# Performance work log

Hardware: AMD Instinct MI355X
Metric: run time of the kernel (lower is better)

The kernel has to match this reference:

```python
import jax, jax.numpy as jnp
import numpy as np

N = 50000      # num_nodes
E = 600000     # num_edges
DIN = 3
D = 128        # hidden_dim == output_dim
H = 4          # heads
C = D // H     # per-head channels = 32
L = 3          # num_layers
NEG_SLOPE = 0.2
LN_EPS = 1e-5


def setup_inputs() -> dict:
    key = jax.random.key(0)
    ks = jax.random.split(key, 14)
    s = 1.0 / np.sqrt(D)
    return {
        "x": jax.random.normal(ks[0], (E, DIN), dtype=jnp.float32),
        "edge_index": jax.random.randint(ks[1], (2, E), 0, N, dtype=jnp.int32),
        "W_edge": jax.random.normal(ks[2], (DIN, D), dtype=jnp.float32) / np.sqrt(DIN),
        "b_edge": jnp.zeros((D,), jnp.float32),
        "W_node": jax.random.normal(ks[3], (D, D), dtype=jnp.float32) * s,
        "b_node": jnp.zeros((D,), jnp.float32),
        "lin_w": jax.random.normal(ks[4], (L, D, D), dtype=jnp.float32) * s,   # GATConv lin (bias=False)
        "att_src": jax.random.normal(ks[5], (L, H, C), dtype=jnp.float32) * s,
        "att_dst": jax.random.normal(ks[6], (L, H, C), dtype=jnp.float32) * s,
        "gat_bias": jnp.zeros((L, D), jnp.float32),
        "ln_g": jnp.ones((L, D), jnp.float32),
        "ln_b": jnp.zeros((L, D), jnp.float32),
        "num_nodes": N,
    }


def _layernorm(x, g, b):
    mu = x.mean(-1, keepdims=True)
    var = ((x - mu) ** 2).mean(-1, keepdims=True)
    return (x - mu) * jax.lax.rsqrt(var + LN_EPS) * g + b


def reference(x, edge_index, W_edge, b_edge, W_node, b_node,
              lin_w, att_src, att_dst, gat_bias, ln_g, ln_b, num_nodes):
    n = num_nodes
    row, col = edge_index[0], edge_index[1]

    # Edge -> node scatter-mean init (x has edge features, E != N)
    edge_h = x @ W_edge + b_edge                                   # [E, D]
    h = jax.ops.segment_sum(edge_h, col, num_segments=n)           # [N, D]
    cnt = jax.ops.segment_sum(jnp.ones((E,), x.dtype), col, num_segments=n)
    h = h / jnp.clip(cnt, 1.0)[:, None]
    h = h @ W_node + b_node

    # self-loops (PyG GATConv default add_self_loops=True)
    loop = jnp.arange(n, dtype=row.dtype)
    src = jnp.concatenate([row, loop])                             # [E+N]
    dst = jnp.concatenate([col, loop])

    for i in range(L):
        xh = (h @ lin_w[i]).reshape(n, H, C)                       # [N, H, C]
        a_s = (xh * att_src[i]).sum(-1)                            # [N, H]
        a_d = (xh * att_dst[i]).sum(-1)
        e = jax.nn.leaky_relu(a_s[src] + a_d[dst], NEG_SLOPE)      # [E+N, H]
        # segment softmax over incoming edges per destination node
        m = jax.ops.segment_max(e, dst, num_segments=n)            # [N, H]
        ex = jnp.exp(e - m[dst])
        denom = jax.ops.segment_sum(ex, dst, num_segments=n)       # [N, H]
        alpha = ex / denom[dst]                                    # [E+N, H]
        out = jax.ops.segment_sum(alpha[:, :, None] * xh[src], dst,
                                  num_segments=n)                  # [N, H, C]
        h_new = out.reshape(n, D) + gat_bias[i]
        h_new = _layernorm(h_new, ln_g[i], ln_b[i])
        if i < L - 1:
            h_new = jax.nn.relu(h_new)
        h = h + h_new                                              # residual (dims match)
    return h
```

## Files before the change

kernel.cpp:

```cpp
#include <hip/hip_runtime.h>
#include <hip/hip_bf16.h>
#include <math.h>

#define D 128
#define H 4
#define NEG_SLOPE 0.2f
#define LN_EPS 1e-5f
#define LDA 136
#define LDE 132

using bf16x8 = __attribute__((ext_vector_type(8))) short;
using f32x4  = __attribute__((ext_vector_type(4))) float;

__device__ __forceinline__ float lrelu(float v) {
    return v > 0.f ? v : NEG_SLOPE * v;
}
__device__ __forceinline__ unsigned short bfb(float f) {
    __hip_bfloat16 h = __float2bfloat16(f);
    return *reinterpret_cast<unsigned short*>(&h);
}

__global__ void k_count(const int* __restrict__ ei, int* __restrict__ cnt, int E) {
    int e = blockIdx.x * blockDim.x + threadIdx.x;
    if (e >= E) return;
    atomicAdd(&cnt[ei[E + e]], 1);
}

__global__ void k_scan_part(const int* __restrict__ cnt, int* __restrict__ off,
                            int* __restrict__ bsum, int N) {
    __shared__ int sm[256];
    int i = blockIdx.x * 256 + threadIdx.x;
    int v = (i < N) ? cnt[i] : 0;
    sm[threadIdx.x] = v;
    __syncthreads();
    #pragma unroll
    for (int o = 1; o < 256; o <<= 1) {
        int t = (threadIdx.x >= (unsigned)o) ? sm[threadIdx.x - o] : 0;
        __syncthreads();
        sm[threadIdx.x] += t;
        __syncthreads();
    }
    if (i < N) off[i] = sm[threadIdx.x];
    if (threadIdx.x == 255) bsum[blockIdx.x] = sm[255];
}

__global__ void k_scan_top(int* __restrict__ bsum, int* __restrict__ off,
                           int NB, int N) {
    __shared__ int sm[256];
    int v = (threadIdx.x < (unsigned)NB) ? bsum[threadIdx.x] : 0;
    sm[threadIdx.x] = v;
    __syncthreads();
    #pragma unroll
    for (int o = 1; o < 256; o <<= 1) {
        int t = (threadIdx.x >= (unsigned)o) ? sm[threadIdx.x - o] : 0;
        __syncthreads();
        sm[threadIdx.x] += t;
        __syncthreads();
    }
    if (threadIdx.x < (unsigned)NB) bsum[threadIdx.x] = sm[threadIdx.x] - v;
    if (threadIdx.x == 255) off[N] = sm[255];
}

__global__ void k_scan_add(const int* __restrict__ cnt, int* __restrict__ off,
                           const int* __restrict__ bsum, int N) {
    int i = blockIdx.x * 256 + threadIdx.x;
    if (i < N) off[i] = off[i] - cnt[i] + bsum[blockIdx.x];
}

__global__ void k_fill(const int* __restrict__ ei, const int* __restrict__ off,
                       int* __restrict__ pos, int2* __restrict__ adj2, int E) {
    int e = blockIdx.x * blockDim.x + threadIdx.x;
    if (e >= E) return;
    int dst = ei[E + e];
    int slot = off[dst] + atomicAdd(&pos[dst], 1);
    adj2[slot] = make_int2(ei[e], e);
}

__global__ __launch_bounds__(256) void k_wprep(
        const float* __restrict__ Wn, const float* __restrict__ lw,
        unsigned short* __restrict__ Wt) {
    __shared__ float Wf[32][132];
    int b = blockIdx.x, w = b >> 2, p = b & 3;
    const float* src = (w == 0) ? (Wn + (size_t)p * 32 * D)
                                : (lw + (size_t)(w - 1) * D * D + (size_t)p * 32 * D);
    int tid = threadIdx.x;
    #pragma unroll
    for (int j = 0; j < 4; j++) {
        int i = tid + j * 256;
        int r = i >> 5, q = i & 31;
        float4 v = reinterpret_cast<const float4*>(src)[i];
        *reinterpret_cast<float4*>(&Wf[r][q * 4]) = v;
    }
    __syncthreads();
    int n = tid & 127, ks = (tid >> 7) * 16;
    unsigned short t16[16];
    #pragma unroll
    for (int j = 0; j < 16; j++) t16[j] = bfb(Wf[ks + j][n]);
    unsigned short* dst = Wt + ((size_t)w * D + n) * D + p * 32 + ks;
    *reinterpret_cast<uint4*>(dst) = *reinterpret_cast<uint4*>(t16);
    *reinterpret_cast<uint4*>(dst + 8) = *reinterpret_cast<uint4*>(t16 + 8);
}

template <int MODE>
__global__ __launch_bounds__(256) void k_gemm(
        const float* __restrict__ A, const unsigned short* __restrict__ Wt,
        const float* __restrict__ bias, float* __restrict__ C,
        __hip_bfloat16* __restrict__ xhb, float* __restrict__ a_s,
        float* __restrict__ a_d, const float* __restrict__ att_s,
        const float* __restrict__ att_d,
        const float* __restrict__ x, const int2* __restrict__ adj2,
        const int* __restrict__ off,
        const float* __restrict__ W_edge, const float* __restrict__ b_edge,
        int N) {
    __shared__ __align__(16) unsigned short AsB[64 * LDA];
    __shared__ __align__(16) unsigned short WtB[128 * LDA];
    int tid = threadIdx.x;
    int n0 = blockIdx.x * 64;

    #pragma unroll
    for (int j = 0; j < 8; j++) {
        int ch = tid + j * 256;
        int r = ch >> 4, c = ch & 15;
        uint4 v = *reinterpret_cast<const uint4*>(Wt + (size_t)r * D + c * 8);
        *reinterpret_cast<uint4*>(&WtB[r * LDA + c * 8]) = v;
    }

    if (MODE == 2) {
        __shared__ float rowf[64][4];
        {
            int r = tid >> 2, t4 = tid & 3;
            int n = n0 + r;
            float s0 = 0.f, s1 = 0.f, s2 = 0.f;
            int degv = 0;
            if (n < N) {
                int beg = off[n], end = off[n + 1];
                degv = end - beg;
                for (int p = beg + t4; p < end; p += 4) {
                    const float* xr = x + (size_t)adj2[p].y * 3;
                    s0 += xr[0]; s1 += xr[1]; s2 += xr[2];
                }
            }
            s0 += __shfl_xor(s0, 1); s0 += __shfl_xor(s0, 2);
            s1 += __shfl_xor(s1, 1); s1 += __shfl_xor(s1, 2);
            s2 += __shfl_xor(s2, 1); s2 += __shfl_xor(s2, 2);
            if (t4 == 0)
                *reinterpret_cast<float4*>(rowf[r]) =
                    make_float4(s0, s1, s2, (float)degv);
        }
        __syncthreads();
        #pragma unroll
        for (int j = 0; j < 4; j++) {
            int ch = tid + j * 256;
            int r = ch >> 4, c = ch & 15;
            float4 rv = *reinterpret_cast<float4*>(rowf[r]);
            float cn = rv.w, rc = 1.f / fmaxf(cn, 1.f);
            int d0 = c * 8;
            unsigned short t8[8];
            #pragma unroll
            for (int q = 0; q < 2; q++) {
                float4 we0 = *reinterpret_cast<const float4*>(W_edge + d0 + q * 4);
                float4 we1 = *reinterpret_cast<const float4*>(W_edge + D + d0 + q * 4);
                float4 we2 = *reinterpret_cast<const float4*>(W_edge + 2 * D + d0 + q * 4);
                float4 be  = *reinterpret_cast<const float4*>(b_edge + d0 + q * 4);
                t8[q * 4 + 0] = bfb((rv.x * we0.x + rv.y * we1.x + rv.z * we2.x + cn * be.x) * rc);
                t8[q * 4 + 1] = bfb((rv.x * we0.y + rv.y * we1.y + rv.z * we2.y + cn * be.y) * rc);
                t8[q * 4 + 2] = bfb((rv.x * we0.z + rv.y * we1.z + rv.z * we2.z + cn * be.z) * rc);
                t8[q * 4 + 3] = bfb((rv.x * we0.w + rv.y * we1.w + rv.z * we2.w + cn * be.w) * rc);
            }
            *reinterpret_cast<uint4*>(&AsB[r * LDA + c * 8]) =
                *reinterpret_cast<uint4*>(t8);
        }
    } else {
        #pragma unroll
        for (int j = 0; j < 4; j++) {
            int ch = tid + j * 256;
            int r = ch >> 4, c = ch & 15;
            int n = n0 + r;
            float4 v0 = make_float4(0.f, 0.f, 0.f, 0.f), v1 = v0;
            if (n < N) {
                v0 = reinterpret_cast<const float4*>(A)[(size_t)n * 32 + c * 2];
                v1 = reinterpret_cast<const float4*>(A)[(size_t)n * 32 + c * 2 + 1];
            }
            unsigned short t8[8] = {bfb(v0.x), bfb(v0.y), bfb(v0.z), bfb(v0.w),
                                    bfb(v1.x), bfb(v1.y), bfb(v1.z), bfb(v1.w)};
            *reinterpret_cast<uint4*>(&AsB[r * LDA + c * 8]) =
                *reinterpret_cast<uint4*>(t8);
        }
    }
    __syncthreads();

    int lane = tid & 63, wv = tid >> 6;
    int lrow = lane & 15, lk = lane >> 4;
    f32x4 acc[8];
    #pragma unroll
    for (int ct = 0; ct < 8; ct++) acc[ct] = (f32x4){0.f, 0.f, 0.f, 0.f};
    int arow = wv * 16 + lrow;
    #pragma unroll
    for (int ks = 0; ks < 4; ks++) {
        bf16x8 af = *reinterpret_cast<const bf16x8*>(
            &AsB[arow * LDA + ks * 32 + lk * 8]);
        #pragma unroll
        for (int ct = 0; ct < 8; ct++) {
            bf16x8 bfr = *reinterpret_cast<const bf16x8*>(
                &WtB[(ct * 16 + lrow) * LDA + ks * 32 + lk * 8]);
            acc[ct] = __builtin_amdgcn_mfma_f32_16x16x32_bf16(af, bfr, acc[ct], 0, 0, 0);
        }
    }
    __syncthreads();

    float* Ef = reinterpret_cast<float*>(WtB);
    #pragma unroll
    for (int ct = 0; ct < 8; ct++)
        #pragma unroll
        for (int j = 0; j < 4; j++)
            Ef[(wv * 16 + lk * 4 + j) * LDE + ct * 16 + lrow] = acc[ct][j];
    __syncthreads();

    int tx = tid & 15, ty = tid >> 4;
    int c0 = tx * 8, r0 = ty * 4;
    float o[4][8];
    #pragma unroll
    for (int r = 0; r < 4; r++) {
        float4 v0 = *reinterpret_cast<const float4*>(&Ef[(r0 + r) * LDE + c0]);
        float4 v1 = *reinterpret_cast<const float4*>(&Ef[(r0 + r) * LDE + c0 + 4]);
        o[r][0] = v0.x; o[r][1] = v0.y; o[r][2] = v0.z; o[r][3] = v0.w;
        o[r][4] = v1.x; o[r][5] = v1.y; o[r][6] = v1.z; o[r][7] = v1.w;
    }

    if (MODE == 2) {
        float b[8];
        #pragma unroll
        for (int c = 0; c < 8; c++) b[c] = bias[c0 + c];
        #pragma unroll
        for (int r = 0; r < 4; r++) {
            int n = n0 + r0 + r;
            if (n >= N) continue;
            float4 o0 = make_float4(o[r][0] + b[0], o[r][1] + b[1],
                                    o[r][2] + b[2], o[r][3] + b[3]);
            float4 o1 = make_float4(o[r][4] + b[4], o[r][5] + b[5],
                                    o[r][6] + b[6], o[r][7] + b[7]);
            reinterpret_cast<float4*>(C)[(size_t)n * 32 + tx * 2] = o0;
            reinterpret_cast<float4*>(C)[(size_t)n * 32 + tx * 2 + 1] = o1;
        }
    } else {
        float ats[8], atd[8];
        #pragma unroll
        for (int c = 0; c < 8; c++) { ats[c] = att_s[c0 + c]; atd[c] = att_d[c0 + c]; }
        #pragma unroll
        for (int r = 0; r < 4; r++) {
            int n = n0 + r0 + r;
            union { uint4 v; unsigned short s[8]; } pk;
            #pragma unroll
            for (int c = 0; c < 8; c++) pk.s[c] = bfb(o[r][c]);
            float ps = 0.f, pd = 0.f;
            #pragma unroll
            for (int c = 0; c < 8; c++) { ps += o[r][c] * ats[c]; pd += o[r][c] * atd[c]; }
            ps += __shfl_xor(ps, 1); ps += __shfl_xor(ps, 2);
            pd += __shfl_xor(pd, 1); pd += __shfl_xor(pd, 2);
            if (n < N) {
                *reinterpret_cast<uint4*>(xhb + (size_t)n * D + c0) = pk.v;
                if ((tx & 3) == 0) {
                    a_s[n * H + (tx >> 2)] = ps;
                    a_d[n * H + (tx >> 2)] = pd;
                }
            }
        }
    }
}

__global__ __launch_bounds__(256) void k_gat5(
        const __hip_bfloat16* __restrict__ xhb, const int* __restrict__ off,
        const int2* __restrict__ adj2, const float* __restrict__ a_s,
        const float* __restrict__ a_d, const float* __restrict__ bias,
        const float* __restrict__ g, const float* __restrict__ bln,
        float* __restrict__ h, int N, int do_relu) {
    int wid = threadIdx.x >> 6;
    int lane = threadIdx.x & 63;
    int n = blockIdx.x * 4 + wid;
    if (n >= N) return;

    int cl = lane & 15;
    int sub = lane >> 4;
    int hb = cl >> 2;
    int c0 = cl * 8;

    int beg = off[n], end = off[n + 1];
    int deg = end - beg;
    int items = deg + 1;
    int itp = (items + 3) & ~3;

    float adA = a_d[n * H + hb];
    float den = 0.f;
    float acc[8];
    #pragma unroll
    for (int c = 0; c < 8; c++) acc[c] = 0.f;

    #pragma unroll 4
    for (int pp = sub; pp < itp; pp += 4) {
        int s = (pp < deg) ? adj2[beg + pp].x : n;
        float av = a_s[(size_t)s * H + hb];
        uint4 u = *reinterpret_cast<const uint4*>(xhb + (size_t)s * D + c0);
        float e = lrelu(av + adA);
        float wv = (pp < items) ? __expf(e) : 0.f;
        den += wv;
        float f;
        f = __uint_as_float(u.x << 16);         acc[0] += wv * f;
        f = __uint_as_float(u.x & 0xffff0000u); acc[1] += wv * f;
        f = __uint_as_float(u.y << 16);         acc[2] += wv * f;
        f = __uint_as_float(u.y & 0xffff0000u); acc[3] += wv * f;
        f = __uint_as_float(u.z << 16);         acc[4] += wv * f;
        f = __uint_as_float(u.z & 0xffff0000u); acc[5] += wv * f;
        f = __uint_as_float(u.w << 16);         acc[6] += wv * f;
        f = __uint_as_float(u.w & 0xffff0000u); acc[7] += wv * f;
    }

    #pragma unroll
    for (int c = 0; c < 8; c++) {
        acc[c] += __shfl_xor(acc[c], 16);
        acc[c] += __shfl_xor(acc[c], 32);
    }
    den += __shfl_xor(den, 16);
    den += __shfl_xor(den, 32);
    float rden = 1.0f / den;

    float4 b0 = *reinterpret_cast<const float4*>(bias + c0);
    float4 b1 = *reinterpret_cast<const float4*>(bias + c0 + 4);
    float o[8];
    o[0] = acc[0] * rden + b0.x; o[1] = acc[1] * rden + b0.y;
    o[2] = acc[2] * rden + b0.z; o[3] = acc[3] * rden + b0.w;
    o[4] = acc[4] * rden + b1.x; o[5] = acc[5] * rden + b1.y;
    o[6] = acc[6] * rden + b1.z; o[7] = acc[7] * rden + b1.w;

    float s1 = 0.f;
    #pragma unroll
    for (int c = 0; c < 8; c++) s1 += o[c];
    #pragma unroll
    for (int os = 1; os < 64; os <<= 1) s1 += __shfl_xor(s1, os);
    float mu = s1 * (1.0f / 512.0f);
    float s2 = 0.f;
    #pragma unroll
    for (int c = 0; c < 8; c++) { float dv = o[c] - mu; s2 += dv * dv; }
    #pragma unroll
    for (int os = 1; os < 64; os <<= 1) s2 += __shfl_xor(s2, os);
    float inv = rsqrtf(s2 * (1.0f / 512.0f) + LN_EPS);

    if (sub == 0) {
        float4 g0 = *reinterpret_cast<const float4*>(g + c0);
        float4 g1 = *reinterpret_cast<const float4*>(g + c0 + 4);
        float4 l0 = *reinterpret_cast<const float4*>(bln + c0);
        float4 l1 = *reinterpret_cast<const float4*>(bln + c0 + 4);
        float y[8];
        y[0] = (o[0] - mu) * inv * g0.x + l0.x;
        y[1] = (o[1] - mu) * inv * g0.y + l0.y;
        y[2] = (o[2] - mu) * inv * g0.z + l0.z;
        y[3] = (o[3] - mu) * inv * g0.w + l0.w;
        y[4] = (o[4] - mu) * inv * g1.x + l1.x;
        y[5] = (o[5] - mu) * inv * g1.y + l1.y;
        y[6] = (o[6] - mu) * inv * g1.z + l1.z;
        y[7] = (o[7] - mu) * inv * g1.w + l1.w;
        if (do_relu) {
            #pragma unroll
            for (int c = 0; c < 8; c++) y[c] = fmaxf(y[c], 0.f);
        }
        float4 h0 = *reinterpret_cast<float4*>(h + (size_t)n * D + c0);
        float4 h1 = *reinterpret_cast<float4*>(h + (size_t)n * D + c0 + 4);
        h0.x += y[0]; h0.y += y[1]; h0.z += y[2]; h0.w += y[3];
        h1.x += y[4]; h1.y += y[5]; h1.z += y[6]; h1.w += y[7];
        *reinterpret_cast<float4*>(h + (size_t)n * D + c0) = h0;
        *reinterpret_cast<float4*>(h + (size_t)n * D + c0 + 4) = h1;
    }
}

extern "C" void kernel_launch(void* const* d_in, const int* in_sizes, int n_in,
                              void* d_out, int out_size, void* d_ws, size_t ws_size,
                              hipStream_t stream) {
    const float* x       = (const float*)d_in[0];
    const int*   ei      = (const int*)  d_in[1];
    const float* W_edge  = (const float*)d_in[2];
    const float* b_edge  = (const float*)d_in[3];
    const float* W_node  = (const float*)d_in[4];
    const float* b_node  = (const float*)d_in[5];
    const float* lin_w   = (const float*)d_in[6];
    const float* att_src = (const float*)d_in[7];
    const float* att_dst = (const float*)d_in[8];
    const float* gat_b   = (const float*)d_in[9];
    const float* ln_g    = (const float*)d_in[10];
    const float* ln_b    = (const float*)d_in[11];

    int N = out_size / D;
    int E = in_sizes[1] / 2;
    int NB = (N + 255) / 256;

    char* w = (char*)d_ws;
    auto carve = [&](size_t bytes) {
        void* p = (void*)w;
        w += (bytes + 255) & ~(size_t)255;
        return p;
    };
    int*   cnt  = (int*)  carve((size_t)N * 4);
    int*   pos  = (int*)  carve((size_t)N * 4);
    int*   off  = (int*)  carve((size_t)(N + 1) * 4);
    int2*  adj2 = (int2*) carve((size_t)E * 8);
    int*   bsum = (int*)  carve((size_t)NB * 4);
    float* tmp  = (float*)carve((size_t)N * D * 4);
    float* a_s  = (float*)carve((size_t)N * H * 4);
    float* a_d  = (float*)carve((size_t)N * H * 4);
    unsigned short* Wt = (unsigned short*)carve((size_t)4 * D * D * 2);
    __hip_bfloat16* xhb = (__hip_bfloat16*)tmp;

    float* h = (float*)d_out;

    hipMemsetAsync(cnt, 0, (size_t)N * 4, stream);
    hipMemsetAsync(pos, 0, (size_t)N * 4, stream);

    int tb = 256;
    k_wprep<<<16, 256, 0, stream>>>(W_node, lin_w, Wt);
    k_count<<<(E + tb - 1) / tb, tb, 0, stream>>>(ei, cnt, E);
    k_scan_part<<<NB, 256, 0, stream>>>(cnt, off, bsum, N);
    k_scan_top<<<1, 256, 0, stream>>>(bsum, off, NB, N);
    k_scan_add<<<NB, 256, 0, stream>>>(cnt, off, bsum, N);
    k_fill<<<(E + tb - 1) / tb, tb, 0, stream>>>(ei, off, pos, adj2, E);
    k_gemm<2><<<(N + 63) / 64, 256, 0, stream>>>(
        nullptr, Wt, b_node, h, nullptr, nullptr, nullptr, nullptr, nullptr,
        x, adj2, off, W_edge, b_edge, N);

    for (int i = 0; i < 3; i++) {
        k_gemm<1><<<(N + 63) / 64, 256, 0, stream>>>(
            h, Wt + (size_t)(i + 1) * D * D, nullptr, nullptr,
            xhb, a_s, a_d, att_src + i * D, att_dst + i * D,
            nullptr, nullptr, nullptr, nullptr, nullptr, N);
        k_gat5<<<(N + 3) / 4, 256, 0, stream>>>(
            xhb, off, adj2, a_s, a_d,
            gat_b + i * D, ln_g + i * D, ln_b + i * D,
            h, N, (i < 2) ? 1 : 0);
    }
}
```

Before: 260.2 us.

## Split adjacency into SoA arrays, read GEMM weights from global, widen GAT lanes

The interleaved (src, edge) adjacency array becomes two separate int arrays, so the GAT gather reads only source indices and the init path reads only edge ids. The GEMM no longer stages the weight matrix in LDS and instead loads B fragments directly from global/L2, which shrinks shared memory and should raise occupancy. The GAT kernel now has each lane handle 16 channels with 8 edge groups per wave and 512-thread blocks, so it processes more edges in parallel per node. The risks are redundant global weight loads in the MFMA loop and higher register pressure from the 16-wide accumulators.

```diff
diff --git a/kernel.cpp b/kernel.cpp
--- a/kernel.cpp
+++ b/kernel.cpp
@@ -68,12 +68,14 @@
 }
 
 __global__ void k_fill(const int* __restrict__ ei, const int* __restrict__ off,
-                       int* __restrict__ pos, int2* __restrict__ adj2, int E) {
+                       int* __restrict__ pos, int* __restrict__ adjs,
+                       int* __restrict__ adje, int E) {
     int e = blockIdx.x * blockDim.x + threadIdx.x;
     if (e >= E) return;
     int dst = ei[E + e];
     int slot = off[dst] + atomicAdd(&pos[dst], 1);
-    adj2[slot] = make_int2(ei[e], e);
+    adjs[slot] = ei[e];
+    adje[slot] = e;
 }
 
 __global__ __launch_bounds__(256) void k_wprep(
@@ -108,22 +110,14 @@
         __hip_bfloat16* __restrict__ xhb, float* __restrict__ a_s,
         float* __restrict__ a_d, const float* __restrict__ att_s,
         const float* __restrict__ att_d,
-        const float* __restrict__ x, const int2* __restrict__ adj2,
+        const float* __restrict__ x, const int* __restrict__ adje,
         const int* __restrict__ off,
         const float* __restrict__ W_edge, const float* __restrict__ b_edge,
         int N) {
-    __shared__ __align__(16) unsigned short AsB[64 * LDA];
-    __shared__ __align__(16) unsigned short WtB[128 * LDA];
+    __shared__ __align__(16) float Ef[64 * LDE];
+    unsigned short* AsB = reinterpret_cast<unsigned short*>(Ef);
     int tid = threadIdx.x;
     int n0 = blockIdx.x * 64;
-
-    #pragma unroll
-    for (int j = 0; j < 8; j++) {
-        int ch = tid + j * 256;
-        int r = ch >> 4, c = ch & 15;
-        uint4 v = *reinterpret_cast<const uint4*>(Wt + (size_t)r * D + c * 8);
-        *reinterpret_cast<uint4*>(&WtB[r * LDA + c * 8]) = v;
-    }
 
     if (MODE == 2) {
         __shared__ float rowf[64][4];
@@ -136,7 +130,7 @@
                 int beg = off[n], end = off[n + 1];
                 degv = end - beg;
                 for (int p = beg + t4; p < end; p += 4) {
-                    const float* xr = x + (size_t)adj2[p].y * 3;
+                    const float* xr = x + (size_t)adje[p] * 3;
                     s0 += xr[0]; s1 += xr[1]; s2 += xr[2];
                 }
             }
@@ -202,13 +196,12 @@
         #pragma unroll
         for (int ct = 0; ct < 8; ct++) {
             bf16x8 bfr = *reinterpret_cast<const bf16x8*>(
-                &WtB[(ct * 16 + lrow) * LDA + ks * 32 + lk * 8]);
+                Wt + (size_t)(ct * 16 + lrow) * D + ks * 32 + lk * 8);
             acc[ct] = __builtin_amdgcn_mfma_f32_16x16x32_bf16(af, bfr, acc[ct], 0, 0, 0);
         }
     }
     __syncthreads();
 
-    float* Ef = reinterpret_cast<float*>(WtB);
     #pragma unroll
     for (int ct = 0; ct < 8; ct++)
         #pragma unroll
@@ -268,106 +261,113 @@
     }
 }
 
-__global__ __launch_bounds__(256) void k_gat5(
+__global__ __launch_bounds__(512) void k_gat6(
         const __hip_bfloat16* __restrict__ xhb, const int* __restrict__ off,
-        const int2* __restrict__ adj2, const float* __restrict__ a_s,
+        const int* __restrict__ adjs, const float* __restrict__ a_s,
         const float* __restrict__ a_d, const float* __restrict__ bias,
         const float* __restrict__ g, const float* __restrict__ bln,
         float* __restrict__ h, int N, int do_relu) {
     int wid = threadIdx.x >> 6;
     int lane = threadIdx.x & 63;
-    int n = blockIdx.x * 4 + wid;
+    int n = blockIdx.x * 8 + wid;
     if (n >= N) return;
 
-    int cl = lane & 15;
-    int sub = lane >> 4;
-    int hb = cl >> 2;
-    int c0 = cl * 8;
+    int cl = lane & 7;
+    int sub = lane >> 3;
+    int hb = cl >> 1;
+    int c0 = cl * 16;
 
     int beg = off[n], end = off[n + 1];
     int deg = end - beg;
     int items = deg + 1;
-    int itp = (items + 3) & ~3;
+    int itp = (items + 7) & ~7;
 
     float adA = a_d[n * H + hb];
     float den = 0.f;
-    float acc[8];
-    #pragma unroll
-    for (int c = 0; c < 8; c++) acc[c] = 0.f;
-
-    #pragma unroll 4
-    for (int pp = sub; pp < itp; pp += 4) {
-        int s = (pp < deg) ? adj2[beg + pp].x : n;
+    float acc[16];
+    #pragma unroll
+    for (int c = 0; c < 16; c++) acc[c] = 0.f;
+
+    #pragma unroll 2
+    for (int pp = sub; pp < itp; pp += 8) {
+        int s = (pp < deg) ? adjs[beg + pp] : n;
         float av = a_s[(size_t)s * H + hb];
-        uint4 u = *reinterpret_cast<const uint4*>(xhb + (size_t)s * D + c0);
+        const uint4* row = reinterpret_cast<const uint4*>(xhb + (size_t)s * D + c0);
+        uint4 u0 = row[0];
+        uint4 u1 = row[1];
         float e = lrelu(av + adA);
         float wv = (pp < items) ? __expf(e) : 0.f;
         den += wv;
         float f;
-        f = __uint_as_float(u.x << 16);         acc[0] += wv * f;
-        f = __uint_as_float(u.x & 0xffff0000u); acc[1] += wv * f;
-        f = __uint_as_float(u.y << 16);         acc[2] += wv * f;
-        f = __uint_as_float(u.y & 0xffff0000u); acc[3] += wv * f;
-        f = __uint_as_float(u.z << 16);         acc[4] += wv * f;
-        f = __uint_as_float(u.z & 0xffff0000u); acc[5] += wv * f;
-        f = __uint_as_float(u.w << 16);         acc[6] += wv * f;
-        f = __uint_as_float(u.w & 0xffff0000u); acc[7] += wv * f;
-    }
-
-    #pragma unroll
-    for (int c = 0; c < 8; c++) {
+        f = __uint_as_float(u0.x << 16);         acc[0]  += wv * f;
+        f = __uint_as_float(u0.x & 0xffff0000u); acc[1]  += wv * f;
+        f = __uint_as_float(u0.y << 16);         acc[2]  += wv * f;
+        f = __uint_as_float(u0.y & 0xffff0000u); acc[3]  += wv * f;
+        f = __uint_as_float(u0.z << 16);         acc[4]  += wv * f;
+        f = __uint_as_float(u0.z & 0xffff0000u); acc[5]  += wv * f;
+        f = __uint_as_float(u0.w << 16);         acc[6]  += wv * f;
+        f = __uint_as_float(u0.w & 0xffff0000u); acc[7]  += wv * f;
+        f = __uint_as_float(u1.x << 16);         acc[8]  += wv * f;
+        f = __uint_as_float(u1.x & 0xffff0000u); acc[9]  += wv * f;
+        f = __uint_as_float(u1.y << 16);         acc[10] += wv * f;
+        f = __uint_as_float(u1.y & 0xffff0000u); acc[11] += wv * f;
+        f = __uint_as_float(u1.z << 16);         acc[12] += wv * f;
+        f = __uint_as_float(u1.z & 0xffff0000u); acc[13] += wv * f;
+        f = __uint_as_float(u1.w << 16);         acc[14] += wv * f;
+        f = __uint_as_float(u1.w & 0xffff0000u); acc[15] += wv * f;
+    }
+
+    #pragma unroll
+    for (int c = 0; c < 16; c++) {
+        acc[c] += __shfl_xor(acc[c], 8);
         acc[c] += __shfl_xor(acc[c], 16);
         acc[c] += __shfl_xor(acc[c], 32);
     }
+    den += __shfl_xor(den, 8);
     den += __shfl_xor(den, 16);
     den += __shfl_xor(den, 32);
     float rden = 1.0f / den;
 
-    float4 b0 = *reinterpret_cast<const float4*>(bias + c0);
-    float4 b1 = *reinterpret_cast<const float4*>(bias + c0 + 4);
-    float o[8];
-    o[0] = acc[0] * rden + b0.x; o[1] = acc[1] * rden + b0.y;
-    o[2] = acc[2] * rden + b0.z; o[3] = acc[3] * rden + b0.w;
-    o[4] = acc[4] * rden + b1.x; o[5] = acc[5] * rden + b1.y;
-    o[6] = acc[6] * rden + b1.z; o[7] = acc[7] * rden + b1.w;
+    float o[16];
+    #pragma unroll
+    for (int q = 0; q < 4; q++) {
+        float4 bq = *reinterpret_cast<const float4*>(bias + c0 + q * 4);
+        o[q * 4 + 0] = acc[q * 4 + 0] * rden + bq.x;
+        o[q * 4 + 1] = acc[q * 4 + 1] * rden + bq.y;
+        o[q * 4 + 2] = acc[q * 4 + 2] * rden + bq.z;
+        o[q * 4 + 3] = acc[q * 4 + 3] * rden + bq.w;
+    }
 
     float s1 = 0.f;
     #pragma unroll
-    for (int c = 0; c < 8; c++) s1 += o[c];
+    for (int c = 0; c < 16; c++) s1 += o[c];
     #pragma unroll
     for (int os = 1; os < 64; os <<= 1) s1 += __shfl_xor(s1, os);
-    float mu = s1 * (1.0f / 512.0f);
+    float mu = s1 * (1.0f / 1024.0f);
     float s2 = 0.f;
     #pragma unroll
-    for (int c = 0; c < 8; c++) { float dv = o[c] - mu; s2 += dv * dv; }
+    for (int c = 0; c < 16; c++) { float dv = o[c] - mu; s2 += dv * dv; }
     #pragma unroll
     for (int os = 1; os < 64; os <<= 1) s2 += __shfl_xor(s2, os);
-    float inv = rsqrtf(s2 * (1.0f / 512.0f) + LN_EPS);
+    float inv = rsqrtf(s2 * (1.0f / 1024.0f) + LN_EPS);
 
     if (sub == 0) {
-        float4 g0 = *reinterpret_cast<const float4*>(g + c0);
-        float4 g1 = *reinterpret_cast<const float4*>(g + c0 + 4);
-        float4 l0 = *reinterpret_cast<const float4*>(bln + c0);
-        float4 l1 = *reinterpret_cast<const float4*>(bln + c0 + 4);
-        float y[8];
-        y[0] = (o[0] - mu) * inv * g0.x + l0.x;
-        y[1] = (o[1] - mu) * inv * g0.y + l0.y;
-        y[2] = (o[2] - mu) * inv * g0.z + l0.z;
-        y[3] = (o[3] - mu) * inv * g0.w + l0.w;
-        y[4] = (o[4] - mu) * inv * g1.x + l1.x;
-        y[5] = (o[5] - mu) * inv * g1.y + l1.y;
-        y[6] = (o[6] - mu) * inv * g1.z + l1.z;
-        y[7] = (o[7] - mu) * inv * g1.w + l1.w;
-        if (do_relu) {
-            #pragma unroll
-            for (int c = 0; c < 8; c++) y[c] = fmaxf(y[c], 0.f);
-        }
-        float4 h0 = *reinterpret_cast<float4*>(h + (size_t)n * D + c0);
-        float4 h1 = *reinterpret_cast<float4*>(h + (size_t)n * D + c0 + 4);
-        h0.x += y[0]; h0.y += y[1]; h0.z += y[2]; h0.w += y[3];
-        h1.x += y[4]; h1.y += y[5]; h1.z += y[6]; h1.w += y[7];
-        *reinterpret_cast<float4*>(h + (size_t)n * D + c0) = h0;
-        *reinterpret_cast<float4*>(h + (size_t)n * D + c0 + 4) = h1;
+        #pragma unroll
+        for (int q = 0; q < 4; q++) {
+            float4 gq = *reinterpret_cast<const float4*>(g + c0 + q * 4);
+            float4 lq = *reinterpret_cast<const float4*>(bln + c0 + q * 4);
+            float y0 = (o[q * 4 + 0] - mu) * inv * gq.x + lq.x;
+            float y1 = (o[q * 4 + 1] - mu) * inv * gq.y + lq.y;
+            float y2 = (o[q * 4 + 2] - mu) * inv * gq.z + lq.z;
+            float y3 = (o[q * 4 + 3] - mu) * inv * gq.w + lq.w;
+            if (do_relu) {
+                y0 = fmaxf(y0, 0.f); y1 = fmaxf(y1, 0.f);
+                y2 = fmaxf(y2, 0.f); y3 = fmaxf(y3, 0.f);
+            }
+            float4 hv = *reinterpret_cast<float4*>(h + (size_t)n * D + c0 + q * 4);
+            hv.x += y0; hv.y += y1; hv.z += y2; hv.w += y3;
+            *reinterpret_cast<float4*>(h + (size_t)n * D + c0 + q * 4) = hv;
+        }
     }
 }
 
@@ -400,7 +400,8 @@
     int*   cnt  = (int*)  carve((size_t)N * 4);
     int*   pos  = (int*)  carve((size_t)N * 4);
     int*   off  = (int*)  carve((size_t)(N + 1) * 4);
-    int2*  adj2 = (int2*) carve((size_t)E * 8);
+    int*   adjs = (int*)  carve((size_t)E * 4);
+    int*   adje = (int*)  carve((size_t)E * 4);
     int*   bsum = (int*)  carve((size_t)NB * 4);
     float* tmp  = (float*)carve((size_t)N * D * 4);
     float* a_s  = (float*)carve((size_t)N * H * 4);
@@ -419,18 +420,18 @@
     k_scan_part<<<NB, 256, 0, stream>>>(cnt, off, bsum, N);
     k_scan_top<<<1, 256, 0, stream>>>(bsum, off, NB, N);
     k_scan_add<<<NB, 256, 0, stream>>>(cnt, off, bsum, N);
-    k_fill<<<(E + tb - 1) / tb, tb, 0, stream>>>(ei, off, pos, adj2, E);
+    k_fill<<<(E + tb - 1) / tb, tb, 0, stream>>>(ei, off, pos, adjs, adje, E);
     k_gemm<2><<<(N + 63) / 64, 256, 0, stream>>>(
         nullptr, Wt, b_node, h, nullptr, nullptr, nullptr, nullptr, nullptr,
-        x, adj2, off, W_edge, b_edge, N);
+        x, adje, off, W_edge, b_edge, N);
 
     for (int i = 0; i < 3; i++) {
         k_gemm<1><<<(N + 63) / 64, 256, 0, stream>>>(
             h, Wt + (size_t)(i + 1) * D * D, nullptr, nullptr,
             xhb, a_s, a_d, att_src + i * D, att_dst + i * D,
             nullptr, nullptr, nullptr, nullptr, nullptr, N);
-        k_gat5<<<(N + 3) / 4, 256, 0, stream>>>(
-            xhb, off, adj2, a_s, a_d,
+        k_gat6<<<(N + 7) / 8, 512, 0, stream>>>(
+            xhb, off, adjs, a_s, a_d,
             gat_b + i * D, ln_g + i * D, ln_b + i * D,
             h, N, (i < 2) ? 1 : 0);
     }
```

After: 331.9 us. +27.6%, slower.
